# Optimization experiments

Hardware: AMD Instinct MI355X
Metric: run time of the kernel (lower is better)

## Reference

```python
import jax, jax.numpy as jnp
import numpy as np
from jax import lax

KS = 3
PAD = 1


def setup_inputs() -> dict:
    key = jax.random.key(0)
    k1, k2, k3 = jax.random.split(key, 3)
    b, c, h, w = 8, 64, 128, 128
    out_c = 64
    x = jax.random.normal(k1, (b, c, h, w), dtype=jnp.float32)
    # small offset weights keep predicted offsets in a sane range
    w_off = jax.random.normal(k2, (2 * KS * KS, c, KS, KS), dtype=jnp.float32) * 0.05
    b_off = jnp.zeros((2 * KS * KS,), dtype=jnp.float32)
    w_reg = jax.random.normal(k3, (out_c, c * KS * KS), dtype=jnp.float32) * 0.02
    b_reg = jnp.zeros((out_c,), dtype=jnp.float32)
    return {"x": x, "w_off": w_off, "b_off": b_off, "w_reg": w_reg, "b_reg": b_reg}


def _deform_forward(x, w_off, b_off, w_reg, b_reg):
    ks, pad = KS, PAD
    b, c, h, w = x.shape
    # offset conv: 3x3, stride 1, pad 1 -> [b, 2*ks*ks, h, w]
    offset = lax.conv_general_dilated(
        x, w_off, window_strides=(1, 1), padding=[(pad, pad), (pad, pad)],
        dimension_numbers=("NCHW", "OIHW", "NCHW"))
    offset = offset + b_off[None, :, None, None]

    # pad input (zeros), as in the torch module
    xp = jnp.pad(x, ((0, 0), (0, 0), (pad, pad), (pad, pad)))
    Hp, Wp = h + 2 * pad, w + 2 * pad

    dt = x.dtype
    # base grid p0: [...,0] = column (x), [...,1] = row (y)
    yy, xx = jnp.meshgrid(jnp.arange(h, dtype=dt), jnp.arange(w, dtype=dt), indexing="ij")
    # kernel offsets p_n: flattened k = i*ks + j -> (lin[j], lin[i])
    lin = jnp.linspace(-(ks - 1) // 2, (ks - 1) // 2, ks).astype(dt)
    pn_i, pn_j = jnp.meshgrid(lin, lin, indexing="ij")
    pn = jnp.stack([pn_j, pn_i], axis=-1).reshape(ks * ks, 2)  # [ks2, 2]

    # offsets: [b, ks2, 2, h, w] -> [b, ks2, h, w, 2]; [...,0]=x off, [...,1]=y off
    off = offset.reshape(b, ks * ks, 2, h, w).transpose(0, 1, 3, 4, 2)

    px = xx[None, None] + pn[None, :, 0, None, None] + off[..., 0]  # [b, ks2, h, w]
    py = yy[None, None] + pn[None, :, 1, None, None] + off[..., 1]

    # torch normalizes by UNPADDED (w-1, h-1) but samples the PADDED tensor with
    # align_corners=True; reproduce exactly: q = p/(dim-1) * (dim_pad-1)
    qx = px / (w - 1) * (Wp - 1)
    qy = py / (h - 1) * (Hp - 1)

    x0 = jnp.floor(qx)
    y0 = jnp.floor(qy)
    wx1 = qx - x0  # frac weights
    wy1 = qy - y0
    wx0 = 1.0 - wx1
    wy0 = 1.0 - wy1
    ix0 = x0.astype(jnp.int32)
    iy0 = y0.astype(jnp.int32)
    ix1 = ix0 + 1
    iy1 = iy0 + 1

    def corner(iy, ix):
        valid = ((iy >= 0) & (iy < Hp) & (ix >= 0) & (ix < Wp)).astype(dt)
        iyc = jnp.clip(iy, 0, Hp - 1)
        ixc = jnp.clip(ix, 0, Wp - 1)
        # gather per batch: img [c,Hp,Wp], idx [ks2,h,w] -> [c,ks2,h,w]
        vals = jax.vmap(lambda img, a, bb: img[:, a, bb])(xp, iyc, ixc)
        return vals * valid[:, None]  # broadcast over channel dim

    v00 = corner(iy0, ix0)
    v01 = corner(iy0, ix1)
    v10 = corner(iy1, ix0)
    v11 = corner(iy1, ix1)

    wy0e = wy0[:, None]; wy1e = wy1[:, None]
    wx0e = wx0[:, None]; wx1e = wx1[:, None]
    sampled = (v00 * wy0e * wx0e + v01 * wy0e * wx1e +
               v10 * wy1e * wx0e + v11 * wy1e * wx1e)  # [b, c, ks2, h, w]

    # layout matches torch: [b, c*ks2, h, w] with (c, kk) order
    xs = sampled.reshape(b, c * ks * ks, h, w)
    out = jnp.einsum("bkhw,ok->bohw", xs, w_reg) + b_reg[None, :, None, None]
    return out


def reference(x, w_off, b_off, w_reg, b_reg):
    return _deform_forward(x, w_off, b_off, w_reg, b_reg)
```

## Files before the change

kernel.cpp:

```cpp
#include <hip/hip_runtime.h>
#include <math.h>

#define HH 128
#define WW 128
#define CC 64
#define BB 8
#define OC 64
#define OFFC 18
#define HW (HH*WW)
#define HP 136
#define WP 136
#define PHW (HP*WP)

typedef __attribute__((ext_vector_type(8))) _Float16 f16x8;
typedef __attribute__((ext_vector_type(4))) float f32x4;

#define P_OFF      0
#define P_SIZE     (BB*32*PHW)
#define OFFS_OFF   (P_OFF + P_SIZE)
#define OFFS_SIZE  (BB*OFFC*HW)
#define WAREG_OFF  (OFFS_OFF + OFFS_SIZE)
#define WAREG_SIZE 18432
#define WAOFF_OFF  (WAREG_OFF + WAREG_SIZE)

#define PAD_BLOCKS 4624
#define PREP_BLOCKS 144

__device__ __forceinline__ unsigned short f2h(float f) {
    _Float16 t = (_Float16)f;
    unsigned short s;
    __builtin_memcpy(&s, &t, 2);
    return s;
}
__device__ __forceinline__ f16x8 u4_to_h8(uint4 u) {
    union { uint4 u; f16x8 h; } c; c.u = u; return c.h;
}
__device__ __forceinline__ uint4 h8_to_u4(f16x8 h) {
    union { uint4 u; f16x8 h; } c; c.h = h; return c.u;
}
__device__ __forceinline__ f16x8 splat8(float f) {
    _Float16 t = (_Float16)f;
    return (f16x8){t, t, t, t, t, t, t, t};
}

__global__ __launch_bounds__(256) void prep_pad_kernel(
    const float* __restrict__ x, uint4* __restrict__ P,
    const float* __restrict__ w_reg, const float* __restrict__ w_off,
    unsigned short* __restrict__ wA_reg, unsigned short* __restrict__ wA_off)
{
    int bid = blockIdx.x;
    int tid = threadIdx.x;
    if (bid < PAD_BLOCKS) {
        int idx = bid * 256 + tid;
        int pos = idx % PHW;
        int ig  = idx / PHW;
        int r   = pos / WP;
        int col = pos % WP;
        union { uint4 u; f16x8 h; } cv;
        cv.u = make_uint4(0u, 0u, 0u, 0u);
        if (r >= 4 && r <= 131 && col >= 4 && col <= 131) {
            const float* src = x + (ig * 8) * HW + (r - 4) * WW + (col - 4);
            #pragma unroll
            for (int e = 0; e < 8; ++e)
                cv.h[e] = (_Float16)src[e * HW];
        }
        P[idx] = cv.u;
    } else {
        int i = (bid - PAD_BLOCKS) * 256 + tid;
        if (i < 18 * 64 * 32) {
            int j = i & 7, quad = (i >> 3) & 3, o = (i >> 5) & 63, ks = i >> 11;
            int kt = ks >> 1, kk = ks & 1;
            int c = kk * 32 + quad * 8 + j;
            wA_reg[i] = f2h(w_reg[o * 576 + c * 9 + kt]);
        }
        if (i < 18 * 32 * 32) {
            int j = i & 7, quad = (i >> 3) & 3, o = (i >> 5) & 31, ks = i >> 10;
            int kt = ks >> 1, kk = ks & 1;
            int c = kk * 32 + quad * 8 + j;
            float v = (o < OFFC) ? w_off[(o * CC + c) * 9 + kt] : 0.0f;
            wA_off[i] = f2h(v);
        }
    }
}

struct Gather8 {
    uint4 a00, a01, a10, a11;
    uint4 b00, b01, b10, b11;
    float wx1, wy1;
};

__device__ __forceinline__ Gather8 issue_tap(
    const uint4* __restrict__ xq0, const uint4* __restrict__ xq1,
    int wv, int hv, int dx, int dy, float offx, float offy)
{
    const float scale = 129.0f / 127.0f;
    float pxf = ((float)wv + (float)dx) + offx;
    float pyf = ((float)hv + (float)dy) + offy;
    float qx = fminf(fmaxf(pxf * scale, -100.0f), 300.0f);
    float qy = fminf(fmaxf(pyf * scale, -100.0f), 300.0f);
    float x0f = floorf(qx), y0f = floorf(qy);
    Gather8 g;
    g.wx1 = qx - x0f;
    g.wy1 = qy - y0f;
    int ix0 = (int)x0f, iy0 = (int)y0f;
    int c0 = min(max(ix0 + 3, 0), WP - 2);
    int r0 = min(max(iy0 + 3, 0), HP - 1);
    int r1 = min(max(iy0 + 4, 0), HP - 1);
    int pr0 = r0 * WP + c0, pr1 = r1 * WP + c0;
    g.a00 = xq0[pr0]; g.a01 = xq0[pr0 + 1];
    g.a10 = xq0[pr1]; g.a11 = xq0[pr1 + 1];
    g.b00 = xq1[pr0]; g.b01 = xq1[pr0 + 1];
    g.b10 = xq1[pr1]; g.b11 = xq1[pr1 + 1];
    return g;
}

__device__ __forceinline__ void blend_write(
    uint4* __restrict__ dst, int qp, int pxl, const Gather8& g)
{
    f16x8 wx1v = splat8(g.wx1), wx0v = splat8(1.0f - g.wx1);
    f16x8 wy1v = splat8(g.wy1), wy0v = splat8(1.0f - g.wy1);
    f16x8 r0a = u4_to_h8(g.a00) * wx0v + u4_to_h8(g.a01) * wx1v;
    f16x8 r1a = u4_to_h8(g.a10) * wx0v + u4_to_h8(g.a11) * wx1v;
    dst[(qp * 2 + 0) * 64 + pxl] = h8_to_u4(r0a * wy0v + r1a * wy1v);
    f16x8 r0b = u4_to_h8(g.b00) * wx0v + u4_to_h8(g.b01) * wx1v;
    f16x8 r1b = u4_to_h8(g.b10) * wx0v + u4_to_h8(g.b11) * wx1v;
    dst[(qp * 2 + 1) * 64 + pxl] = h8_to_u4(r0b * wy0v + r1b * wy1v);
}

__global__ __launch_bounds__(256, 7) void fused_deform_kernel(
    const uint4* __restrict__ P, const unsigned short* __restrict__ wA_off,
    const float* __restrict__ b_off, const unsigned short* __restrict__ wA_reg,
    const float* __restrict__ b_reg, float* __restrict__ out)
{
    __shared__ uint4 shbuf[1024];
    __shared__ float offs_lds[OFFC * 64];
    int img  = blockIdx.x & 7;
    int rest = blockIdx.x >> 3;
    int half = rest & 1;
    int pblk = rest >> 1;
    int tid  = threadIdx.x;
    int pxl  = tid & 63;
    int qp   = tid >> 6;
    int lane = tid & 63;
    int wvid = tid >> 6;
    int wv = half * 64 + pxl;
    int hv = pblk;

    {
        int s2  = wvid & 1;
        int ph2 = wvid >> 1;
        const f16x8* wOv = (const f16x8*)wA_off;
        f32x4 oacc[2];
        oacc[0] = (f32x4){0.f, 0.f, 0.f, 0.f};
        oacc[1] = (f32x4){0.f, 0.f, 0.f, 0.f};
        for (int kk = 0; kk < 2; ++kk) {
            for (int i = tid; i < 3 * 4 * 66; i += 256) {
                int r   = i / 264;
                int rem = i - r * 264;
                int gl  = rem / 66;
                int j   = rem - gl * 66;
                shbuf[(r * 4 + gl) * 66 + j] =
                    P[(img * 8 + kk * 4 + gl) * PHW + (pblk + 3 + r) * WP + (half * 64 + 3 + j)];
            }
            __syncthreads();
            const f16x8* xsc = (const f16x8*)shbuf;
            for (int tap = 0; tap < 9; ++tap) {
                int dy = tap / 3, dx = tap % 3;
                f16x8 a = wOv[((tap * 2 + kk) * 32 + s2 * 16 + (lane & 15)) * 4 + (lane >> 4)];
                #pragma unroll
                for (int pt = 0; pt < 2; ++pt) {
                    int sj = ph2 * 32 + pt * 16 + (lane & 15) + dx;
                    f16x8 b = xsc[(dy * 4 + (lane >> 4)) * 66 + sj];
                    oacc[pt] = __builtin_amdgcn_mfma_f32_16x16x32_f16(a, b, oacc[pt], 0, 0, 0);
                }
            }
            __syncthreads();
        }
        #pragma unroll
        for (int r = 0; r < 4; ++r) {
            int o = s2 * 16 + (lane >> 4) * 4 + r;
            if (o < OFFC) {
                float bias = b_off[o];
                #pragma unroll
                for (int pt = 0; pt < 2; ++pt) {
                    int p = ph2 * 32 + pt * 16 + (lane & 15);
                    offs_lds[o * 64 + p] = oacc[pt][r] + bias;
                }
            }
        }
    }
    __syncthreads();

    const f16x8* wAv = (const f16x8*)wA_reg;
    const uint4* xq0 = P + (img * 8 + qp * 2 + 0) * PHW;
    const uint4* xq1 = P + (img * 8 + qp * 2 + 1) * PHW;
    int aidx = (wvid * 16 + (lane & 15)) * 4 + (lane >> 4);

    f32x4 acc[4];
    #pragma unroll
    for (int pt = 0; pt < 4; ++pt) acc[pt] = (f32x4){0.f, 0.f, 0.f, 0.f};

    for (int tap = 0; tap < 9; ++tap) {
        float ox = offs_lds[(2 * tap + 0) * 64 + pxl];
        float oy = offs_lds[(2 * tap + 1) * 64 + pxl];
        f16x8 a0c = wAv[(tap * 2 + 0) * 256 + aidx];
        f16x8 a1c = wAv[(tap * 2 + 1) * 256 + aidx];

        Gather8 cur = issue_tap(xq0, xq1, wv, hv, tap % 3 - 1, tap / 3 - 1, ox, oy);
        uint4* dst = shbuf + (tap & 1) * 512;
        blend_write(dst, qp, pxl, cur);
        __syncthreads();

        const f16x8* xsv = (const f16x8*)(shbuf + (tap & 1) * 512);
        #pragma unroll
        for (int pt = 0; pt < 4; ++pt) {
            int pxi = pt * 16 + (lane & 15);
            f16x8 b0 = xsv[(lane >> 4) * 64 + pxi];
            acc[pt] = __builtin_amdgcn_mfma_f32_16x16x32_f16(a0c, b0, acc[pt], 0, 0, 0);
            f16x8 b1 = xsv[(4 + (lane >> 4)) * 64 + pxi];
            acc[pt] = __builtin_amdgcn_mfma_f32_16x16x32_f16(a1c, b1, acc[pt], 0, 0, 0);
        }
    }

    float* op = out + img * (OC * HW) + hv * WW + half * 64;
    #pragma unroll
    for (int r = 0; r < 4; ++r) {
        int o = wvid * 16 + (lane >> 4) * 4 + r;
        float bias = b_reg[o];
        #pragma unroll
        for (int pt = 0; pt < 4; ++pt)
            op[o * HW + pt * 16 + (lane & 15)] = acc[pt][r] + bias;
    }
}

extern "C" void kernel_launch(void* const* d_in, const int* in_sizes, int n_in,
                              void* d_out, int out_size, void* d_ws, size_t ws_size,
                              hipStream_t stream) {
    const float* x     = (const float*)d_in[0];
    const float* w_off = (const float*)d_in[1];
    const float* b_off = (const float*)d_in[2];
    const float* w_reg = (const float*)d_in[3];
    const float* b_reg = (const float*)d_in[4];
    float* out = (float*)d_out;
    float* ws  = (float*)d_ws;

    uint4* P      = (uint4*)(ws + P_OFF);
    unsigned short* wA_reg = (unsigned short*)(ws + WAREG_OFF);
    unsigned short* wA_off = (unsigned short*)(ws + WAOFF_OFF);

    prep_pad_kernel<<<PAD_BLOCKS + PREP_BLOCKS, 256, 0, stream>>>(
        x, P, w_reg, w_off, wA_reg, wA_off);
    fused_deform_kernel<<<2048, 256, 0, stream>>>(
        P, wA_off, b_off, wA_reg, b_reg, out);
}
```

Baseline: 179.4 us.

## Feed bilinear samples directly into MFMA B operand, dropping LDS staging

Each wave now owns 16 pixels across all 64 output channels. It computes the bilinear blend in registers arranged to match the MFMA B-operand layout and feeds it straight into the matrix instructions, which removes the per-tap LDS write, the __syncthreads barrier and the LDS reread. The weight A operands are loaded per output tile inside the tap loop. The launch-bounds occupancy hint drops from 7 to 4 blocks per CU. Each lane still gathers 2 channel-groups x 4 corners per tap, but the gathers now stride across channel groups. Weight loads from global/L2 rise fourfold per tap.

New measurement: 194.8 us. 1.09x slower.

```diff
diff --git a/kernel.cpp b/kernel.cpp
--- a/kernel.cpp
+++ b/kernel.cpp
@@ -34,9 +34,6 @@
 }
 __device__ __forceinline__ f16x8 u4_to_h8(uint4 u) {
     union { uint4 u; f16x8 h; } c; c.u = u; return c.h;
-}
-__device__ __forceinline__ uint4 h8_to_u4(f16x8 h) {
-    union { uint4 u; f16x8 h; } c; c.h = h; return c.u;
 }
 __device__ __forceinline__ f16x8 splat8(float f) {
     _Float16 t = (_Float16)f;
@@ -114,36 +111,20 @@
     return g;
 }
 
-__device__ __forceinline__ void blend_write(
-    uint4* __restrict__ dst, int qp, int pxl, const Gather8& g)
-{
-    f16x8 wx1v = splat8(g.wx1), wx0v = splat8(1.0f - g.wx1);
-    f16x8 wy1v = splat8(g.wy1), wy0v = splat8(1.0f - g.wy1);
-    f16x8 r0a = u4_to_h8(g.a00) * wx0v + u4_to_h8(g.a01) * wx1v;
-    f16x8 r1a = u4_to_h8(g.a10) * wx0v + u4_to_h8(g.a11) * wx1v;
-    dst[(qp * 2 + 0) * 64 + pxl] = h8_to_u4(r0a * wy0v + r1a * wy1v);
-    f16x8 r0b = u4_to_h8(g.b00) * wx0v + u4_to_h8(g.b01) * wx1v;
-    f16x8 r1b = u4_to_h8(g.b10) * wx0v + u4_to_h8(g.b11) * wx1v;
-    dst[(qp * 2 + 1) * 64 + pxl] = h8_to_u4(r0b * wy0v + r1b * wy1v);
-}
-
-__global__ __launch_bounds__(256, 7) void fused_deform_kernel(
+__global__ __launch_bounds__(256, 4) void fused_deform_kernel(
     const uint4* __restrict__ P, const unsigned short* __restrict__ wA_off,
     const float* __restrict__ b_off, const unsigned short* __restrict__ wA_reg,
     const float* __restrict__ b_reg, float* __restrict__ out)
 {
-    __shared__ uint4 shbuf[1024];
+    __shared__ uint4 shbuf[3 * 4 * 66];
     __shared__ float offs_lds[OFFC * 64];
     int img  = blockIdx.x & 7;
     int rest = blockIdx.x >> 3;
     int half = rest & 1;
     int pblk = rest >> 1;
     int tid  = threadIdx.x;
-    int pxl  = tid & 63;
-    int qp   = tid >> 6;
     int lane = tid & 63;
     int wvid = tid >> 6;
-    int wv = half * 64 + pxl;
     int hv = pblk;
 
     {
@@ -192,44 +173,48 @@
     __syncthreads();
 
     const f16x8* wAv = (const f16x8*)wA_reg;
-    const uint4* xq0 = P + (img * 8 + qp * 2 + 0) * PHW;
-    const uint4* xq1 = P + (img * 8 + qp * 2 + 1) * PHW;
-    int aidx = (wvid * 16 + (lane & 15)) * 4 + (lane >> 4);
+    int pxi  = lane & 15;
+    int cg   = lane >> 4;
+    int wvpx = wvid * 16 + pxi;
+    int wcol = half * 64 + wvpx;
+    const uint4* xqA = P + (img * 8 + cg) * PHW;
+    const uint4* xqB = P + (img * 8 + cg + 4) * PHW;
 
     f32x4 acc[4];
     #pragma unroll
-    for (int pt = 0; pt < 4; ++pt) acc[pt] = (f32x4){0.f, 0.f, 0.f, 0.f};
+    for (int ot = 0; ot < 4; ++ot) acc[ot] = (f32x4){0.f, 0.f, 0.f, 0.f};
 
     for (int tap = 0; tap < 9; ++tap) {
-        float ox = offs_lds[(2 * tap + 0) * 64 + pxl];
-        float oy = offs_lds[(2 * tap + 1) * 64 + pxl];
-        f16x8 a0c = wAv[(tap * 2 + 0) * 256 + aidx];
-        f16x8 a1c = wAv[(tap * 2 + 1) * 256 + aidx];
-
-        Gather8 cur = issue_tap(xq0, xq1, wv, hv, tap % 3 - 1, tap / 3 - 1, ox, oy);
-        uint4* dst = shbuf + (tap & 1) * 512;
-        blend_write(dst, qp, pxl, cur);
-        __syncthreads();
-
-        const f16x8* xsv = (const f16x8*)(shbuf + (tap & 1) * 512);
+        float ox = offs_lds[(2 * tap + 0) * 64 + wvpx];
+        float oy = offs_lds[(2 * tap + 1) * 64 + wvpx];
+        Gather8 g = issue_tap(xqA, xqB, wcol, hv, tap % 3 - 1, tap / 3 - 1, ox, oy);
+
+        f16x8 wx1v = splat8(g.wx1), wx0v = splat8(1.0f - g.wx1);
+        f16x8 wy1v = splat8(g.wy1), wy0v = splat8(1.0f - g.wy1);
+        f16x8 r0a = u4_to_h8(g.a00) * wx0v + u4_to_h8(g.a01) * wx1v;
+        f16x8 r1a = u4_to_h8(g.a10) * wx0v + u4_to_h8(g.a11) * wx1v;
+        f16x8 B0  = r0a * wy0v + r1a * wy1v;
+        f16x8 r0b = u4_to_h8(g.b00) * wx0v + u4_to_h8(g.b01) * wx1v;
+        f16x8 r1b = u4_to_h8(g.b10) * wx0v + u4_to_h8(g.b11) * wx1v;
+        f16x8 B1  = r0b * wy0v + r1b * wy1v;
+
         #pragma unroll
-        for (int pt = 0; pt < 4; ++pt) {
-            int pxi = pt * 16 + (lane & 15);
-            f16x8 b0 = xsv[(lane >> 4) * 64 + pxi];
-            acc[pt] = __builtin_amdgcn_mfma_f32_16x16x32_f16(a0c, b0, acc[pt], 0, 0, 0);
-            f16x8 b1 = xsv[(4 + (lane >> 4)) * 64 + pxi];
-            acc[pt] = __builtin_amdgcn_mfma_f32_16x16x32_f16(a1c, b1, acc[pt], 0, 0, 0);
-        }
-    }
-
-    float* op = out + img * (OC * HW) + hv * WW + half * 64;
+        for (int ot = 0; ot < 4; ++ot) {
+            f16x8 a0 = wAv[((tap * 2 + 0) * 64 + ot * 16 + pxi) * 4 + cg];
+            f16x8 a1 = wAv[((tap * 2 + 1) * 64 + ot * 16 + pxi) * 4 + cg];
+            acc[ot] = __builtin_amdgcn_mfma_f32_16x16x32_f16(a0, B0, acc[ot], 0, 0, 0);
+            acc[ot] = __builtin_amdgcn_mfma_f32_16x16x32_f16(a1, B1, acc[ot], 0, 0, 0);
+        }
+    }
+
+    float* op = out + img * (OC * HW) + hv * WW + half * 64 + wvid * 16;
     #pragma unroll
-    for (int r = 0; r < 4; ++r) {
-        int o = wvid * 16 + (lane >> 4) * 4 + r;
-        float bias = b_reg[o];
+    for (int ot = 0; ot < 4; ++ot) {
         #pragma unroll
-        for (int pt = 0; pt < 4; ++pt)
-            op[o * HW + pt * 16 + (lane & 15)] = acc[pt][r] + bias;
+        for (int r = 0; r < 4; ++r) {
+            int o = ot * 16 + cg * 4 + r;
+            op[o * HW + pxi] = acc[ot][r] + b_reg[o];
+        }
     }
 }
 
```
